# Kernel tuning notes

Hardware: AMD Instinct MI355X
Metric: run time of the kernel (lower is better)

Reference implementation:

```python
import jax, jax.numpy as jnp
import numpy as np

N_NODES = 100000
N_EDGES = 1600000
D = 128
D_FF = 2 * D
BN_EPS = 1e-5


def setup_inputs() -> dict:
    key = jax.random.key(0)
    ks = jax.random.split(key, 16)
    s = lambda k, shp, fan: jax.random.normal(k, shp, jnp.float32) / np.float32(np.sqrt(fan))
    return {
        "x": jax.random.normal(ks[0], (N_NODES, D), jnp.float32),
        "edge_attr": jax.random.normal(ks[1], (N_EDGES, D), jnp.float32),
        "w1g": s(ks[2], (D, D), D),
        "b1g": jnp.zeros((D,), jnp.float32),
        "w2g": s(ks[3], (D, D), D),
        "b2g": jnp.zeros((D,), jnp.float32),
        "bn1_g": jax.random.uniform(ks[4], (D,), jnp.float32, 0.5, 1.5),
        "bn1_b": 0.1 * jax.random.normal(ks[5], (D,), jnp.float32),
        "ff_w1": s(ks[6], (D, D_FF), D),
        "ff_b1": jnp.zeros((D_FF,), jnp.float32),
        "ff_w2": s(ks[7], (D_FF, D), D_FF),
        "ff_b2": jnp.zeros((D,), jnp.float32),
        "bn2_g": jax.random.uniform(ks[8], (D,), jnp.float32, 0.5, 1.5),
        "bn2_b": 0.1 * jax.random.normal(ks[9], (D,), jnp.float32),
        "edge_index": jax.random.randint(ks[10], (2, N_EDGES), 0, N_NODES, jnp.int64 if jax.config.jax_enable_x64 else jnp.int32),
    }


def _batchnorm(h, gamma, beta):
    # training-mode BatchNorm1d: per-batch (node-axis) stats, biased variance
    mean = h.mean(axis=0)
    var = ((h - mean) ** 2).mean(axis=0)
    return gamma * (h - mean) * jax.lax.rsqrt(var + BN_EPS) + beta


def reference(x, edge_attr, w1g, b1g, w2g, b2g, bn1_g, bn1_b,
              ff_w1, ff_b1, ff_w2, ff_b2, bn2_g, bn2_b, edge_index):
    src, dst = edge_index[0], edge_index[1]
    # GINEConv message: relu(x_j + e_ij), scatter-sum into target nodes
    msg = jax.nn.relu(x[src] + edge_attr)                      # [E, D]
    agg = jax.ops.segment_sum(msg, dst, num_segments=N_NODES)  # [N, D]
    h = x + agg                                                # (1+eps)*x with eps=0
    # gin_nn: Linear -> ReLU -> Linear
    h = jax.nn.relu(h @ w1g + b1g) @ w2g + b2g
    h = jax.nn.relu(h)                                         # post-conv relu; dropout=identity (eval)
    h = x + h                                                  # residual
    h = _batchnorm(h, bn1_g, bn1_b)                            # norm1_local
    ff = jax.nn.relu(h @ ff_w1 + ff_b1) @ ff_w2 + ff_b2        # FFN block (dropouts identity)
    h = h + ff
    h = _batchnorm(h, bn2_g, bn2_b)                            # norm2
    return h
```

## Files before the change

kernel.cpp:

```cpp
#include <hip/hip_runtime.h>
#include <hip/hip_bf16.h>

#define NN 100000
#define NE 1600000
#define DD 128
#define DFF 256
#define BN_EPS 1e-5f
#define NND ((size_t)NN * DD)
#define NB_SCAN 391
#define NTILE 6250

typedef __attribute__((ext_vector_type(8))) short short8;
typedef __attribute__((ext_vector_type(4))) float f32x4;
typedef __attribute__((ext_vector_type(4))) unsigned short us4;

static __device__ __forceinline__ unsigned short f2bf(float f) {
  union { float f; unsigned u; } v; v.f = f;
  unsigned r = v.u + 0x7fffu + ((v.u >> 16) & 1u);
  return (unsigned short)(r >> 16);
}
static __device__ __forceinline__ float bf2f(unsigned short h) {
  union { unsigned u; float f; } v; v.u = ((unsigned)h) << 16;
  return v.f;
}

__global__ __launch_bounds__(256) void k_prep_misc(const float* __restrict__ x,
    unsigned short* __restrict__ xbf,
    const float* __restrict__ w1g, const float* __restrict__ w2g,
    const float* __restrict__ ffw1, const float* __restrict__ ffw2,
    unsigned short* __restrict__ w1t, unsigned short* __restrict__ w2t,
    unsigned short* __restrict__ fw1t, unsigned short* __restrict__ fw2t) {
  int b = blockIdx.x;
  if (b < 6250) {
    size_t base = ((size_t)b * 256u + threadIdx.x) * 8;
    const f32x4* xp = reinterpret_cast<const f32x4*>(x + base);
    f32x4 a0 = xp[0], a1 = xp[1];
    short8 o;
#pragma unroll
    for (int j = 0; j < 4; ++j) o[j] = (short)f2bf(a0[j]);
#pragma unroll
    for (int j = 0; j < 4; ++j) o[4 + j] = (short)f2bf(a1[j]);
    *reinterpret_cast<short8*>(xbf + base) = o;
  } else {
    int i = (b - 6250) * 256 + threadIdx.x;
    if (i < 16384) { int c = i & 127, k = i >> 7; w1t[c * 128 + k] = f2bf(w1g[k * 128 + c]); }
    else if (i < 32768) { i -= 16384; int c = i & 127, k = i >> 7; w2t[c * 128 + k] = f2bf(w2g[k * 128 + c]); }
    else if (i < 65536) { i -= 32768; int c = i & 255, k = i >> 8; fw1t[c * 128 + k] = f2bf(ffw1[k * 256 + c]); }
    else if (i < 98304) { i -= 65536; int c = i & 127, k = i >> 7; fw2t[c * 256 + k] = f2bf(ffw2[k * 128 + c]); }
  }
}

__global__ __launch_bounds__(256) void k_hist(const int* __restrict__ ei,
                                              int* __restrict__ cnt) {
  int e = blockIdx.x * 256 + threadIdx.x;
  if (e >= NE) return;
  atomicAdd(&cnt[ei[NE + e]], 1);
}

__global__ __launch_bounds__(256) void k_scan1(const int* __restrict__ cnt,
                                               int* __restrict__ bsum) {
  __shared__ int sh[256];
  int n = blockIdx.x * 256 + threadIdx.x;
  sh[threadIdx.x] = (n < NN) ? cnt[n] : 0;
  __syncthreads();
  for (int off = 128; off > 0; off >>= 1) {
    if (threadIdx.x < off) sh[threadIdx.x] += sh[threadIdx.x + off];
    __syncthreads();
  }
  if (threadIdx.x == 0) bsum[blockIdx.x] = sh[0];
}

__global__ __launch_bounds__(512) void k_scan2(const int* __restrict__ bsum,
                                               int* __restrict__ bpre,
                                               int* __restrict__ rs) {
  __shared__ int sh[512];
  int t = threadIdx.x;
  int v = (t < NB_SCAN) ? bsum[t] : 0;
  sh[t] = v;
  __syncthreads();
  for (int off = 1; off < 512; off <<= 1) {
    int u = (t >= off) ? sh[t - off] : 0;
    __syncthreads();
    sh[t] += u;
    __syncthreads();
  }
  if (t < NB_SCAN) bpre[t] = sh[t] - v;
  if (t == NB_SCAN - 1) rs[NN] = sh[t];
}

__global__ __launch_bounds__(256) void k_scan3(int* __restrict__ rs,
                                               const int* __restrict__ bpre,
                                               int* __restrict__ cursor) {
  __shared__ int sh[256];
  int n = blockIdx.x * 256 + threadIdx.x;
  int t = threadIdx.x;
  int v = (n < NN) ? rs[n] : 0;
  sh[t] = v;
  __syncthreads();
  for (int off = 1; off < 256; off <<= 1) {
    int u = (t >= off) ? sh[t - off] : 0;
    __syncthreads();
    sh[t] += u;
    __syncthreads();
  }
  if (n < NN) {
    int ex = bpre[blockIdx.x] + sh[t] - v;
    rs[n] = ex;
    cursor[n] = ex;
  }
}

__global__ __launch_bounds__(256) void k_scatter(const int* __restrict__ ei,
                                                 int* __restrict__ cursor,
                                                 int2* __restrict__ el2) {
  int e = blockIdx.x * 256 + threadIdx.x;
  if (e >= NE) return;
  int s = ei[e], d = ei[NE + e];
  int p = atomicAdd(&cursor[d], 1);
  el2[p] = make_int2(e, s);
}

__global__ __launch_bounds__(256) void k_gather(
    const unsigned short* __restrict__ xbf, const float* __restrict__ ea,
    const int* __restrict__ rs, const int2* __restrict__ el2,
    unsigned short* __restrict__ h0) {
  int n = blockIdx.x * 8 + (threadIdx.x >> 5);
  int q = threadIdx.x & 31;
  int beg = rs[n], end = rs[n + 1];
  f32x4 acc = (f32x4){0.f, 0.f, 0.f, 0.f};
  int2 E0 = make_int2(0, 0), E1 = E0, E2 = E0, E3 = E0;
  int i = beg;
  if (i     < end) E0 = el2[i];
  if (i + 1 < end) E1 = el2[i + 1];
  if (i + 2 < end) E2 = el2[i + 2];
  if (i + 3 < end) E3 = el2[i + 3];
  for (; i + 4 <= end; i += 4) {
    f32x4 ev0 = *(reinterpret_cast<const f32x4*>(ea + (size_t)E0.x * DD) + q);
    us4  xv0 = *reinterpret_cast<const us4*>(xbf + (size_t)E0.y * DD + q * 4);
    f32x4 ev1 = *(reinterpret_cast<const f32x4*>(ea + (size_t)E1.x * DD) + q);
    us4  xv1 = *reinterpret_cast<const us4*>(xbf + (size_t)E1.y * DD + q * 4);
    f32x4 ev2 = *(reinterpret_cast<const f32x4*>(ea + (size_t)E2.x * DD) + q);
    us4  xv2 = *reinterpret_cast<const us4*>(xbf + (size_t)E2.y * DD + q * 4);
    f32x4 ev3 = *(reinterpret_cast<const f32x4*>(ea + (size_t)E3.x * DD) + q);
    us4  xv3 = *reinterpret_cast<const us4*>(xbf + (size_t)E3.y * DD + q * 4);
    int2 N0 = E0, N1 = E1, N2 = E2, N3 = E3;
    if (i + 4 < end) N0 = el2[i + 4];
    if (i + 5 < end) N1 = el2[i + 5];
    if (i + 6 < end) N2 = el2[i + 6];
    if (i + 7 < end) N3 = el2[i + 7];
#pragma unroll
    for (int c = 0; c < 4; ++c) {
      float m0 = bf2f((unsigned short)xv0[c]) + ev0[c];
      acc[c] += (m0 > 0.f) ? m0 : 0.f;
      float m1 = bf2f((unsigned short)xv1[c]) + ev1[c];
      acc[c] += (m1 > 0.f) ? m1 : 0.f;
      float m2 = bf2f((unsigned short)xv2[c]) + ev2[c];
      acc[c] += (m2 > 0.f) ? m2 : 0.f;
      float m3 = bf2f((unsigned short)xv3[c]) + ev3[c];
      acc[c] += (m3 > 0.f) ? m3 : 0.f;
    }
    E0 = N0; E1 = N1; E2 = N2; E3 = N3;
  }
  if (i < end) {
    f32x4 ev = *(reinterpret_cast<const f32x4*>(ea + (size_t)E0.x * DD) + q);
    us4  xv = *reinterpret_cast<const us4*>(xbf + (size_t)E0.y * DD + q * 4);
#pragma unroll
    for (int c = 0; c < 4; ++c) {
      float m = bf2f((unsigned short)xv[c]) + ev[c];
      acc[c] += (m > 0.f) ? m : 0.f;
    }
  }
  if (i + 1 < end) {
    f32x4 ev = *(reinterpret_cast<const f32x4*>(ea + (size_t)E1.x * DD) + q);
    us4  xv = *reinterpret_cast<const us4*>(xbf + (size_t)E1.y * DD + q * 4);
#pragma unroll
    for (int c = 0; c < 4; ++c) {
      float m = bf2f((unsigned short)xv[c]) + ev[c];
      acc[c] += (m > 0.f) ? m : 0.f;
    }
  }
  if (i + 2 < end) {
    f32x4 ev = *(reinterpret_cast<const f32x4*>(ea + (size_t)E2.x * DD) + q);
    us4  xv = *reinterpret_cast<const us4*>(xbf + (size_t)E2.y * DD + q * 4);
#pragma unroll
    for (int c = 0; c < 4; ++c) {
      float m = bf2f((unsigned short)xv[c]) + ev[c];
      acc[c] += (m > 0.f) ? m : 0.f;
    }
  }
  us4 xs = *reinterpret_cast<const us4*>(xbf + (size_t)n * DD + q * 4);
  union { unsigned short us[4]; unsigned long long u; } pk;
#pragma unroll
  for (int c = 0; c < 4; ++c) pk.us[c] = f2bf(bf2f((unsigned short)xs[c]) + acc[c]);
  *reinterpret_cast<unsigned long long*>(h0 + (size_t)n * DD + q * 4) = pk.u;
}

#define TR1 136
__global__ __launch_bounds__(256) void k_mlp1(const unsigned short* __restrict__ A,
    const unsigned short* __restrict__ W1T, const float* __restrict__ b1,
    const unsigned short* __restrict__ W2T, const float* __restrict__ b2,
    const float* __restrict__ x, float* __restrict__ O, float* __restrict__ stats) {
  __shared__ unsigned short tr[4][16 * TR1];
  __shared__ float lds_s[128], lds_q[128];
  if (threadIdx.x < 128) { lds_s[threadIdx.x] = 0.f; lds_q[threadIdx.x] = 0.f; }
  int lane = threadIdx.x & 63, w = threadIdx.x >> 6;
  int tile = blockIdx.x * 4 + w;
  int l15 = lane & 15, g = lane >> 4;
  int row0 = tile * 16;
  __syncthreads();
  if (tile < NTILE) {
    f32x4 acc[8];
#pragma unroll
    for (int ct = 0; ct < 8; ++ct) {
      float b = b1[ct * 16 + l15];
      acc[ct] = (f32x4){b, b, b, b};
    }
    short8 a[4];
#pragma unroll
    for (int kt = 0; kt < 4; ++kt)
      a[kt] = *reinterpret_cast<const short8*>(A + (size_t)(row0 + l15) * DD + kt * 32 + g * 8);
#pragma unroll
    for (int kt = 0; kt < 4; ++kt) {
      int k0 = kt * 32 + g * 8;
#pragma unroll
      for (int ct = 0; ct < 8; ++ct) {
        int c = ct * 16 + l15;
        short8 b = *reinterpret_cast<const short8*>(W1T + (size_t)c * DD + k0);
        acc[ct] = __builtin_amdgcn_mfma_f32_16x16x32_bf16(a[kt], b, acc[ct], 0, 0, 0);
      }
    }
#pragma unroll
    for (int ct = 0; ct < 8; ++ct) {
#pragma unroll
      for (int r = 0; r < 4; ++r) {
        float v = acc[ct][r];
        v = v > 0.f ? v : 0.f;
        tr[w][(g * 4 + r) * TR1 + ct * 16 + l15] = f2bf(v);
      }
    }
  }
  __syncthreads();
  if (tile < NTILE) {
    short8 a2[4];
#pragma unroll
    for (int kt = 0; kt < 4; ++kt)
      a2[kt] = *reinterpret_cast<const short8*>(&tr[w][l15 * TR1 + kt * 32 + g * 8]);
    f32x4 acc2[8];
#pragma unroll
    for (int ct = 0; ct < 8; ++ct) {
      float b = b2[ct * 16 + l15];
      acc2[ct] = (f32x4){b, b, b, b};
    }
#pragma unroll
    for (int kt = 0; kt < 4; ++kt) {
      int k0 = kt * 32 + g * 8;
#pragma unroll
      for (int ct = 0; ct < 8; ++ct) {
        int c = ct * 16 + l15;
        short8 b = *reinterpret_cast<const short8*>(W2T + (size_t)c * DD + k0);
        acc2[ct] = __builtin_amdgcn_mfma_f32_16x16x32_bf16(a2[kt], b, acc2[ct], 0, 0, 0);
      }
    }
#pragma unroll
    for (int ct = 0; ct < 8; ++ct) {
      int c = ct * 16 + l15;
      float s = 0.f, q = 0.f;
#pragma unroll
      for (int r = 0; r < 4; ++r) {
        int row = row0 + g * 4 + r;
        float v = acc2[ct][r];
        v = v > 0.f ? v : 0.f;
        v += x[(size_t)row * DD + c];
        O[(size_t)row * DD + c] = v;
        s += v; q += v * v;
      }
      s += __shfl_xor(s, 16); s += __shfl_xor(s, 32);
      q += __shfl_xor(q, 16); q += __shfl_xor(q, 32);
      if (g == 0) { atomicAdd(&lds_s[c], s); atomicAdd(&lds_q[c], q); }
    }
  }
  __syncthreads();
  if (threadIdx.x < 128) {
    atomicAdd(&stats[threadIdx.x], lds_s[threadIdx.x]);
    atomicAdd(&stats[128 + threadIdx.x], lds_q[threadIdx.x]);
  }
}

__global__ void k_bnfin(const float* __restrict__ st, const float* __restrict__ gm,
                        const float* __restrict__ bt, float* __restrict__ par) {
  int c = threadIdx.x;
  float mean = st[c] * (1.f / NN);
  float var = st[128 + c] * (1.f / NN) - mean * mean;
  float sc = gm[c] * rsqrtf(var + BN_EPS);
  par[c] = sc;
  par[128 + c] = bt[c] - mean * sc;
}

#define TR2 264
__global__ __launch_bounds__(256) void k_mlp2(const float* __restrict__ H,
    const float* __restrict__ par, const unsigned short* __restrict__ FW1T,
    const float* __restrict__ fb1, const unsigned short* __restrict__ FW2T,
    const float* __restrict__ fb2, float* __restrict__ O, float* __restrict__ stats) {
  __shared__ unsigned short tr[4][16 * TR2];
  __shared__ float lds_s[128], lds_q[128];
  if (threadIdx.x < 128) { lds_s[threadIdx.x] = 0.f; lds_q[threadIdx.x] = 0.f; }
  int lane = threadIdx.x & 63, w = threadIdx.x >> 6;
  int tile = blockIdx.x * 4 + w;
  int l15 = lane & 15, g = lane >> 4;
  int row0 = tile * 16;
  __syncthreads();
  if (tile < NTILE) {
    const float* arow = H + (size_t)(row0 + l15) * DD;
    short8 a1[4];
#pragma unroll
    for (int kt = 0; kt < 4; ++kt) {
      int k0 = kt * 32 + g * 8;
      f32x4 u0 = *reinterpret_cast<const f32x4*>(arow + k0);
      f32x4 u1 = *reinterpret_cast<const f32x4*>(arow + k0 + 4);
      f32x4 sc0 = *reinterpret_cast<const f32x4*>(par + k0);
      f32x4 sc1 = *reinterpret_cast<const f32x4*>(par + k0 + 4);
      f32x4 sh0 = *reinterpret_cast<const f32x4*>(par + 128 + k0);
      f32x4 sh1 = *reinterpret_cast<const f32x4*>(par + 128 + k0 + 4);
      short8 af;
#pragma unroll
      for (int j = 0; j < 4; ++j) af[j] = (short)f2bf(sc0[j] * u0[j] + sh0[j]);
#pragma unroll
      for (int j = 0; j < 4; ++j) af[4 + j] = (short)f2bf(sc1[j] * u1[j] + sh1[j]);
      a1[kt] = af;
    }
    f32x4 acc1[16];
#pragma unroll
    for (int ct = 0; ct < 16; ++ct) {
      float b = fb1[ct * 16 + l15];
      acc1[ct] = (f32x4){b, b, b, b};
    }
#pragma unroll
    for (int kt = 0; kt < 4; ++kt) {
      int k0 = kt * 32 + g * 8;
#pragma unroll
      for (int ct = 0; ct < 16; ++ct) {
        int c = ct * 16 + l15;
        short8 b = *reinterpret_cast<const short8*>(FW1T + (size_t)c * DD + k0);
        acc1[ct] = __builtin_amdgcn_mfma_f32_16x16x32_bf16(a1[kt], b, acc1[ct], 0, 0, 0);
      }
    }
#pragma unroll
    for (int ct = 0; ct < 16; ++ct) {
#pragma unroll
      for (int r = 0; r < 4; ++r) {
        float v = acc1[ct][r];
        v = v > 0.f ? v : 0.f;
        tr[w][(g * 4 + r) * TR2 + ct * 16 + l15] = f2bf(v);
      }
    }
  }
  __syncthreads();
  if (tile < NTILE) {
    short8 a2[8];
#pragma unroll
    for (int kt = 0; kt < 8; ++kt)
      a2[kt] = *reinterpret_cast<const short8*>(&tr[w][l15 * TR2 + kt * 32 + g * 8]);
    f32x4 acc2[8];
#pragma unroll
    for (int ct = 0; ct < 8; ++ct) {
      float b = fb2[ct * 16 + l15];
      acc2[ct] = (f32x4){b, b, b, b};
    }
#pragma unroll 2
    for (int kt = 0; kt < 8; ++kt) {
      int k0 = kt * 32 + g * 8;
#pragma unroll
      for (int ct = 0; ct < 8; ++ct) {
        int c = ct * 16 + l15;
        short8 b = *reinterpret_cast<const short8*>(FW2T + (size_t)c * DFF + k0);
        acc2[ct] = __builtin_amdgcn_mfma_f32_16x16x32_bf16(a2[kt], b, acc2[ct], 0, 0, 0);
      }
    }
#pragma unroll
    for (int ct = 0; ct < 8; ++ct) {
      int c = ct * 16 + l15;
      float sc = par[c], sh = par[128 + c];
      float s = 0.f, q = 0.f;
#pragma unroll
      for (int r = 0; r < 4; ++r) {
        int row = row0 + g * 4 + r;
        float h1v = sc * O[(size_t)row * DD + c] + sh;
        float v = acc2[ct][r] + h1v;
        O[(size_t)row * DD + c] = v;
        s += v; q += v * v;
      }
      s += __shfl_xor(s, 16); s += __shfl_xor(s, 32);
      q += __shfl_xor(q, 16); q += __shfl_xor(q, 32);
      if (g == 0) { atomicAdd(&lds_s[c], s); atomicAdd(&lds_q[c], q); }
    }
  }
  __syncthreads();
  if (threadIdx.x < 128) {
    atomicAdd(&stats[threadIdx.x], lds_s[threadIdx.x]);
    atomicAdd(&stats[128 + threadIdx.x], lds_q[threadIdx.x]);
  }
}

__global__ __launch_bounds__(256) void k_bnfinal(float* __restrict__ h,
    const float* __restrict__ st, const float* __restrict__ gm,
    const float* __restrict__ bt) {
  size_t base = ((size_t)blockIdx.x * 256u + threadIdx.x) * 4;
  int c0 = (int)(base & 127);
  f32x4 v = *reinterpret_cast<f32x4*>(h + base);
#pragma unroll
  for (int j = 0; j < 4; ++j) {
    int c = c0 + j;
    float mean = st[c] * (1.f / NN);
    float var = st[128 + c] * (1.f / NN) - mean * mean;
    float sc = gm[c] * rsqrtf(var + BN_EPS);
    float sh = bt[c] - mean * sc;
    v[j] = sc * v[j] + sh;
  }
  *reinterpret_cast<f32x4*>(h + base) = v;
}

extern "C" void kernel_launch(void* const* d_in, const int* in_sizes, int n_in,
                              void* d_out, int out_size, void* d_ws, size_t ws_size,
                              hipStream_t stream) {
  const float* x    = (const float*)d_in[0];
  const float* ea   = (const float*)d_in[1];
  const float* w1g  = (const float*)d_in[2];
  const float* b1g  = (const float*)d_in[3];
  const float* w2g  = (const float*)d_in[4];
  const float* b2g  = (const float*)d_in[5];
  const float* bn1g = (const float*)d_in[6];
  const float* bn1b = (const float*)d_in[7];
  const float* ffw1 = (const float*)d_in[8];
  const float* ffb1 = (const float*)d_in[9];
  const float* ffw2 = (const float*)d_in[10];
  const float* ffb2 = (const float*)d_in[11];
  const float* bn2g = (const float*)d_in[12];
  const float* bn2b = (const float*)d_in[13];
  const int*   eidx = (const int*)d_in[14];
  float* out = (float*)d_out;

  char* ws = (char*)d_ws;
  int2* el2    = (int2*)(ws);
  int*  rs     = (int*)(ws + 12800000);
  int*  cursor = (int*)(ws + 13200128);
  int*  bsum   = (int*)(ws + 13600128);
  int*  bpre   = (int*)(ws + 13601728);
  float* stats = (float*)(ws + 13603328);
  float* par   = (float*)(ws + 13605376);
  unsigned short* w1t  = (unsigned short*)(ws + 13607424);
  unsigned short* w2t  = w1t + 16384;
  unsigned short* fw1t = w2t + 16384;
  unsigned short* fw2t = fw1t + 32768;
  unsigned short* xbf  = (unsigned short*)(ws + 13804032);
  unsigned short* hbf  = (unsigned short*)(ws + 39404032);

  hipMemsetAsync(rs, 0, (NN + 1) * 4, stream);
  hipMemsetAsync(stats, 0, 512 * 4, stream);

  k_prep_misc<<<6634, 256, 0, stream>>>(x, xbf, w1g, w2g, ffw1, ffw2,
                                        w1t, w2t, fw1t, fw2t);

  k_hist<<<6250, 256, 0, stream>>>(eidx, rs);
  k_scan1<<<NB_SCAN, 256, 0, stream>>>(rs, bsum);
  k_scan2<<<1, 512, 0, stream>>>(bsum, bpre, rs);
  k_scan3<<<NB_SCAN, 256, 0, stream>>>(rs, bpre, cursor);
  k_scatter<<<6250, 256, 0, stream>>>(eidx, cursor, el2);

  k_gather<<<12500, 256, 0, stream>>>(xbf, ea, rs, el2, hbf);

  k_mlp1<<<1563, 256, 0, stream>>>(hbf, w1t, b1g, w2t, b2g, x, out, stats);
  k_bnfin<<<1, 128, 0, stream>>>(stats, bn1g, bn1b, par);
  k_mlp2<<<1563, 256, 0, stream>>>(out, par, fw1t, ffb1, fw2t, ffb2, out, stats + 256);
  k_bnfinal<<<12500, 256, 0, stream>>>(out, stats + 256, bn2g, bn2b);
}
```

Measured before the change: 722.0 us.

## Stage MLP weights in swizzled LDS, loop tiles per block, fuse hist into prep

The MLP kernels now copy the bf16 weight matrices once per block into LDS with an XOR swizzle, and each wave processes four 16-row tiles. The grid shrinks from 1563 to 391 blocks so the weight load is spread over more work. The histogram kernel is merged into the prep launch, the stats memset moves into k_scan2, and the residual in mlp1 reads bf16 x instead of fp32 x. The costs are higher LDS use (lower occupancy), fewer blocks on the device, and a small precision loss in the residual term.

```diff
diff --git a/kernel.cpp b/kernel.cpp
--- a/kernel.cpp
+++ b/kernel.cpp
@@ -29,7 +29,8 @@
     const float* __restrict__ w1g, const float* __restrict__ w2g,
     const float* __restrict__ ffw1, const float* __restrict__ ffw2,
     unsigned short* __restrict__ w1t, unsigned short* __restrict__ w2t,
-    unsigned short* __restrict__ fw1t, unsigned short* __restrict__ fw2t) {
+    unsigned short* __restrict__ fw1t, unsigned short* __restrict__ fw2t,
+    const int* __restrict__ ei, int* __restrict__ cnt) {
   int b = blockIdx.x;
   if (b < 6250) {
     size_t base = ((size_t)b * 256u + threadIdx.x) * 8;
@@ -41,20 +42,16 @@
 #pragma unroll
     for (int j = 0; j < 4; ++j) o[4 + j] = (short)f2bf(a1[j]);
     *reinterpret_cast<short8*>(xbf + base) = o;
-  } else {
+  } else if (b < 6634) {
     int i = (b - 6250) * 256 + threadIdx.x;
     if (i < 16384) { int c = i & 127, k = i >> 7; w1t[c * 128 + k] = f2bf(w1g[k * 128 + c]); }
     else if (i < 32768) { i -= 16384; int c = i & 127, k = i >> 7; w2t[c * 128 + k] = f2bf(w2g[k * 128 + c]); }
     else if (i < 65536) { i -= 32768; int c = i & 255, k = i >> 8; fw1t[c * 128 + k] = f2bf(ffw1[k * 256 + c]); }
     else if (i < 98304) { i -= 65536; int c = i & 127, k = i >> 7; fw2t[c * 256 + k] = f2bf(ffw2[k * 128 + c]); }
-  }
-}
-
-__global__ __launch_bounds__(256) void k_hist(const int* __restrict__ ei,
-                                              int* __restrict__ cnt) {
-  int e = blockIdx.x * 256 + threadIdx.x;
-  if (e >= NE) return;
-  atomicAdd(&cnt[ei[NE + e]], 1);
+  } else {
+    int e = (b - 6634) * 256 + threadIdx.x;
+    if (e < NE) atomicAdd(&cnt[ei[NE + e]], 1);
+  }
 }
 
 __global__ __launch_bounds__(256) void k_scan1(const int* __restrict__ cnt,
@@ -72,9 +69,11 @@
 
 __global__ __launch_bounds__(512) void k_scan2(const int* __restrict__ bsum,
                                                int* __restrict__ bpre,
-                                               int* __restrict__ rs) {
+                                               int* __restrict__ rs,
+                                               float* __restrict__ stats) {
   __shared__ int sh[512];
   int t = threadIdx.x;
+  stats[t] = 0.f;
   int v = (t < NB_SCAN) ? bsum[t] : 0;
   sh[t] = v;
   __syncthreads();
@@ -199,90 +198,103 @@
 __global__ __launch_bounds__(256) void k_mlp1(const unsigned short* __restrict__ A,
     const unsigned short* __restrict__ W1T, const float* __restrict__ b1,
     const unsigned short* __restrict__ W2T, const float* __restrict__ b2,
-    const float* __restrict__ x, float* __restrict__ O, float* __restrict__ stats) {
+    const unsigned short* __restrict__ xbf, float* __restrict__ O,
+    float* __restrict__ stats) {
+  __shared__ unsigned short w1s[16384];
+  __shared__ unsigned short w2s[16384];
   __shared__ unsigned short tr[4][16 * TR1];
   __shared__ float lds_s[128], lds_q[128];
-  if (threadIdx.x < 128) { lds_s[threadIdx.x] = 0.f; lds_q[threadIdx.x] = 0.f; }
-  int lane = threadIdx.x & 63, w = threadIdx.x >> 6;
-  int tile = blockIdx.x * 4 + w;
+  int t = threadIdx.x;
+  if (t < 128) { lds_s[t] = 0.f; lds_q[t] = 0.f; }
+  {
+    const short8* s1 = reinterpret_cast<const short8*>(W1T);
+    const short8* s2 = reinterpret_cast<const short8*>(W2T);
+    for (int i = t; i < 2048; i += 256) {
+      int byte = i * 16;
+      int c = byte >> 8;
+      int sb = byte ^ ((c & 7) << 4);
+      *reinterpret_cast<short8*>(reinterpret_cast<char*>(w1s) + sb) = s1[i];
+      *reinterpret_cast<short8*>(reinterpret_cast<char*>(w2s) + sb) = s2[i];
+    }
+  }
+  __syncthreads();
+  int lane = t & 63, w = t >> 6;
   int l15 = lane & 15, g = lane >> 4;
-  int row0 = tile * 16;
-  __syncthreads();
-  if (tile < NTILE) {
-    f32x4 acc[8];
-#pragma unroll
-    for (int ct = 0; ct < 8; ++ct) {
-      float b = b1[ct * 16 + l15];
-      acc[ct] = (f32x4){b, b, b, b};
-    }
-    short8 a[4];
-#pragma unroll
-    for (int kt = 0; kt < 4; ++kt)
-      a[kt] = *reinterpret_cast<const short8*>(A + (size_t)(row0 + l15) * DD + kt * 32 + g * 8);
-#pragma unroll
-    for (int kt = 0; kt < 4; ++kt) {
-      int k0 = kt * 32 + g * 8;
+  for (int tt = 0; tt < 4; ++tt) {
+    int tile = blockIdx.x * 16 + w * 4 + tt;
+    bool valid = tile < NTILE;
+    int row0 = tile * 16;
+    if (valid) {
+      short8 a[4];
+#pragma unroll
+      for (int kt = 0; kt < 4; ++kt)
+        a[kt] = *reinterpret_cast<const short8*>(A + (size_t)(row0 + l15) * DD + kt * 32 + g * 8);
+      f32x4 acc[8];
+#pragma unroll
+      for (int ct = 0; ct < 8; ++ct) { float b = b1[ct * 16 + l15]; acc[ct] = (f32x4){b, b, b, b}; }
+#pragma unroll
+      for (int kt = 0; kt < 4; ++kt) {
+        int k0 = kt * 32 + g * 8;
+#pragma unroll
+        for (int ct = 0; ct < 8; ++ct) {
+          int c = ct * 16 + l15;
+          int byte = ((c << 8) + k0 * 2) ^ ((c & 7) << 4);
+          short8 b = *reinterpret_cast<const short8*>(reinterpret_cast<const char*>(w1s) + byte);
+          acc[ct] = __builtin_amdgcn_mfma_f32_16x16x32_bf16(a[kt], b, acc[ct], 0, 0, 0);
+        }
+      }
+#pragma unroll
+      for (int ct = 0; ct < 8; ++ct)
+#pragma unroll
+        for (int r = 0; r < 4; ++r) {
+          float v = acc[ct][r];
+          v = v > 0.f ? v : 0.f;
+          tr[w][(g * 4 + r) * TR1 + ct * 16 + l15] = f2bf(v);
+        }
+    }
+    __syncthreads();
+    if (valid) {
+      short8 a2[4];
+#pragma unroll
+      for (int kt = 0; kt < 4; ++kt)
+        a2[kt] = *reinterpret_cast<const short8*>(&tr[w][l15 * TR1 + kt * 32 + g * 8]);
+      f32x4 acc2[8];
+#pragma unroll
+      for (int ct = 0; ct < 8; ++ct) { float b = b2[ct * 16 + l15]; acc2[ct] = (f32x4){b, b, b, b}; }
+#pragma unroll
+      for (int kt = 0; kt < 4; ++kt) {
+        int k0 = kt * 32 + g * 8;
+#pragma unroll
+        for (int ct = 0; ct < 8; ++ct) {
+          int c = ct * 16 + l15;
+          int byte = ((c << 8) + k0 * 2) ^ ((c & 7) << 4);
+          short8 b = *reinterpret_cast<const short8*>(reinterpret_cast<const char*>(w2s) + byte);
+          acc2[ct] = __builtin_amdgcn_mfma_f32_16x16x32_bf16(a2[kt], b, acc2[ct], 0, 0, 0);
+        }
+      }
 #pragma unroll
       for (int ct = 0; ct < 8; ++ct) {
         int c = ct * 16 + l15;
-        short8 b = *reinterpret_cast<const short8*>(W1T + (size_t)c * DD + k0);
-        acc[ct] = __builtin_amdgcn_mfma_f32_16x16x32_bf16(a[kt], b, acc[ct], 0, 0, 0);
-      }
-    }
-#pragma unroll
-    for (int ct = 0; ct < 8; ++ct) {
-#pragma unroll
-      for (int r = 0; r < 4; ++r) {
-        float v = acc[ct][r];
-        v = v > 0.f ? v : 0.f;
-        tr[w][(g * 4 + r) * TR1 + ct * 16 + l15] = f2bf(v);
-      }
-    }
-  }
-  __syncthreads();
-  if (tile < NTILE) {
-    short8 a2[4];
-#pragma unroll
-    for (int kt = 0; kt < 4; ++kt)
-      a2[kt] = *reinterpret_cast<const short8*>(&tr[w][l15 * TR1 + kt * 32 + g * 8]);
-    f32x4 acc2[8];
-#pragma unroll
-    for (int ct = 0; ct < 8; ++ct) {
-      float b = b2[ct * 16 + l15];
-      acc2[ct] = (f32x4){b, b, b, b};
-    }
-#pragma unroll
-    for (int kt = 0; kt < 4; ++kt) {
-      int k0 = kt * 32 + g * 8;
-#pragma unroll
-      for (int ct = 0; ct < 8; ++ct) {
-        int c = ct * 16 + l15;
-        short8 b = *reinterpret_cast<const short8*>(W2T + (size_t)c * DD + k0);
-        acc2[ct] = __builtin_amdgcn_mfma_f32_16x16x32_bf16(a2[kt], b, acc2[ct], 0, 0, 0);
-      }
-    }
-#pragma unroll
-    for (int ct = 0; ct < 8; ++ct) {
-      int c = ct * 16 + l15;
-      float s = 0.f, q = 0.f;
-#pragma unroll
-      for (int r = 0; r < 4; ++r) {
-        int row = row0 + g * 4 + r;
-        float v = acc2[ct][r];
-        v = v > 0.f ? v : 0.f;
-        v += x[(size_t)row * DD + c];
-        O[(size_t)row * DD + c] = v;
-        s += v; q += v * v;
-      }
-      s += __shfl_xor(s, 16); s += __shfl_xor(s, 32);
-      q += __shfl_xor(q, 16); q += __shfl_xor(q, 32);
-      if (g == 0) { atomicAdd(&lds_s[c], s); atomicAdd(&lds_q[c], q); }
-    }
-  }
-  __syncthreads();
-  if (threadIdx.x < 128) {
-    atomicAdd(&stats[threadIdx.x], lds_s[threadIdx.x]);
-    atomicAdd(&stats[128 + threadIdx.x], lds_q[threadIdx.x]);
+        float s = 0.f, q = 0.f;
+#pragma unroll
+        for (int r = 0; r < 4; ++r) {
+          int row = row0 + g * 4 + r;
+          float v = acc2[ct][r];
+          v = v > 0.f ? v : 0.f;
+          v += bf2f(xbf[(size_t)row * DD + c]);
+          O[(size_t)row * DD + c] = v;
+          s += v; q += v * v;
+        }
+        s += __shfl_xor(s, 16); s += __shfl_xor(s, 32);
+        q += __shfl_xor(q, 16); q += __shfl_xor(q, 32);
+        if (g == 0) { atomicAdd(&lds_s[c], s); atomicAdd(&lds_q[c], q); }
+      }
+    }
+    __syncthreads();
+  }
+  if (t < 128) {
+    atomicAdd(&stats[t], lds_s[t]);
+    atomicAdd(&stats[128 + t], lds_q[t]);
   }
 }
 
@@ -301,103 +313,111 @@
     const float* __restrict__ par, const unsigned short* __restrict__ FW1T,
     const float* __restrict__ fb1, const unsigned short* __restrict__ FW2T,
     const float* __restrict__ fb2, float* __restrict__ O, float* __restrict__ stats) {
+  __shared__ unsigned short fw1s[32768];
   __shared__ unsigned short tr[4][16 * TR2];
   __shared__ float lds_s[128], lds_q[128];
-  if (threadIdx.x < 128) { lds_s[threadIdx.x] = 0.f; lds_q[threadIdx.x] = 0.f; }
-  int lane = threadIdx.x & 63, w = threadIdx.x >> 6;
-  int tile = blockIdx.x * 4 + w;
+  int t = threadIdx.x;
+  if (t < 128) { lds_s[t] = 0.f; lds_q[t] = 0.f; }
+  {
+    const short8* s1 = reinterpret_cast<const short8*>(FW1T);
+    for (int i = t; i < 4096; i += 256) {
+      int byte = i * 16;
+      int c = byte >> 8;
+      int sb = byte ^ ((c & 7) << 4);
+      *reinterpret_cast<short8*>(reinterpret_cast<char*>(fw1s) + sb) = s1[i];
+    }
+  }
+  __syncthreads();
+  int lane = t & 63, w = t >> 6;
   int l15 = lane & 15, g = lane >> 4;
-  int row0 = tile * 16;
-  __syncthreads();
-  if (tile < NTILE) {
-    const float* arow = H + (size_t)(row0 + l15) * DD;
-    short8 a1[4];
-#pragma unroll
-    for (int kt = 0; kt < 4; ++kt) {
-      int k0 = kt * 32 + g * 8;
-      f32x4 u0 = *reinterpret_cast<const f32x4*>(arow + k0);
-      f32x4 u1 = *reinterpret_cast<const f32x4*>(arow + k0 + 4);
-      f32x4 sc0 = *reinterpret_cast<const f32x4*>(par + k0);
-      f32x4 sc1 = *reinterpret_cast<const f32x4*>(par + k0 + 4);
-      f32x4 sh0 = *reinterpret_cast<const f32x4*>(par + 128 + k0);
-      f32x4 sh1 = *reinterpret_cast<const f32x4*>(par + 128 + k0 + 4);
-      short8 af;
-#pragma unroll
-      for (int j = 0; j < 4; ++j) af[j] = (short)f2bf(sc0[j] * u0[j] + sh0[j]);
-#pragma unroll
-      for (int j = 0; j < 4; ++j) af[4 + j] = (short)f2bf(sc1[j] * u1[j] + sh1[j]);
-      a1[kt] = af;
-    }
-    f32x4 acc1[16];
-#pragma unroll
-    for (int ct = 0; ct < 16; ++ct) {
-      float b = fb1[ct * 16 + l15];
-      acc1[ct] = (f32x4){b, b, b, b};
-    }
-#pragma unroll
-    for (int kt = 0; kt < 4; ++kt) {
-      int k0 = kt * 32 + g * 8;
-#pragma unroll
-      for (int ct = 0; ct < 16; ++ct) {
-        int c = ct * 16 + l15;
-        short8 b = *reinterpret_cast<const short8*>(FW1T + (size_t)c * DD + k0);
-        acc1[ct] = __builtin_amdgcn_mfma_f32_16x16x32_bf16(a1[kt], b, acc1[ct], 0, 0, 0);
-      }
-    }
-#pragma unroll
-    for (int ct = 0; ct < 16; ++ct) {
-#pragma unroll
-      for (int r = 0; r < 4; ++r) {
-        float v = acc1[ct][r];
-        v = v > 0.f ? v : 0.f;
-        tr[w][(g * 4 + r) * TR2 + ct * 16 + l15] = f2bf(v);
-      }
-    }
-  }
-  __syncthreads();
-  if (tile < NTILE) {
-    short8 a2[8];
-#pragma unroll
-    for (int kt = 0; kt < 8; ++kt)
-      a2[kt] = *reinterpret_cast<const short8*>(&tr[w][l15 * TR2 + kt * 32 + g * 8]);
-    f32x4 acc2[8];
-#pragma unroll
-    for (int ct = 0; ct < 8; ++ct) {
-      float b = fb2[ct * 16 + l15];
-      acc2[ct] = (f32x4){b, b, b, b};
-    }
+  for (int tt = 0; tt < 4; ++tt) {
+    int tile = blockIdx.x * 16 + w * 4 + tt;
+    bool valid = tile < NTILE;
+    int row0 = tile * 16;
+    if (valid) {
+      const float* arow = H + (size_t)(row0 + l15) * DD;
+      short8 a1[4];
+#pragma unroll
+      for (int kt = 0; kt < 4; ++kt) {
+        int k0 = kt * 32 + g * 8;
+        f32x4 u0 = *reinterpret_cast<const f32x4*>(arow + k0);
+        f32x4 u1 = *reinterpret_cast<const f32x4*>(arow + k0 + 4);
+        f32x4 sc0 = *reinterpret_cast<const f32x4*>(par + k0);
+        f32x4 sc1 = *reinterpret_cast<const f32x4*>(par + k0 + 4);
+        f32x4 sh0 = *reinterpret_cast<const f32x4*>(par + 128 + k0);
+        f32x4 sh1 = *reinterpret_cast<const f32x4*>(par + 128 + k0 + 4);
+        short8 af;
+#pragma unroll
+        for (int j = 0; j < 4; ++j) af[j] = (short)f2bf(sc0[j] * u0[j] + sh0[j]);
+#pragma unroll
+        for (int j = 0; j < 4; ++j) af[4 + j] = (short)f2bf(sc1[j] * u1[j] + sh1[j]);
+        a1[kt] = af;
+      }
+      f32x4 acc1[16];
+#pragma unroll
+      for (int ct = 0; ct < 16; ++ct) { float b = fb1[ct * 16 + l15]; acc1[ct] = (f32x4){b, b, b, b}; }
+#pragma unroll
+      for (int kt = 0; kt < 4; ++kt) {
+        int k0 = kt * 32 + g * 8;
+#pragma unroll
+        for (int ct = 0; ct < 16; ++ct) {
+          int c = ct * 16 + l15;
+          int byte = ((c << 8) + k0 * 2) ^ ((c & 7) << 4);
+          short8 b = *reinterpret_cast<const short8*>(reinterpret_cast<const char*>(fw1s) + byte);
+          acc1[ct] = __builtin_amdgcn_mfma_f32_16x16x32_bf16(a1[kt], b, acc1[ct], 0, 0, 0);
+        }
+      }
+#pragma unroll
+      for (int ct = 0; ct < 16; ++ct)
+#pragma unroll
+        for (int r = 0; r < 4; ++r) {
+          float v = acc1[ct][r];
+          v = v > 0.f ? v : 0.f;
+          tr[w][(g * 4 + r) * TR2 + ct * 16 + l15] = f2bf(v);
+        }
+    }
+    __syncthreads();
+    if (valid) {
+      short8 a2[8];
+#pragma unroll
+      for (int kt = 0; kt < 8; ++kt)
+        a2[kt] = *reinterpret_cast<const short8*>(&tr[w][l15 * TR2 + kt * 32 + g * 8]);
+      f32x4 acc2[8];
+#pragma unroll
+      for (int ct = 0; ct < 8; ++ct) { float b = fb2[ct * 16 + l15]; acc2[ct] = (f32x4){b, b, b, b}; }
 #pragma unroll 2
-    for (int kt = 0; kt < 8; ++kt) {
-      int k0 = kt * 32 + g * 8;
+      for (int kt = 0; kt < 8; ++kt) {
+        int k0 = kt * 32 + g * 8;
+#pragma unroll
+        for (int ct = 0; ct < 8; ++ct) {
+          int c = ct * 16 + l15;
+          short8 b = *reinterpret_cast<const short8*>(FW2T + (size_t)c * DFF + k0);
+          acc2[ct] = __builtin_amdgcn_mfma_f32_16x16x32_bf16(a2[kt], b, acc2[ct], 0, 0, 0);
+        }
+      }
 #pragma unroll
       for (int ct = 0; ct < 8; ++ct) {
         int c = ct * 16 + l15;
-        short8 b = *reinterpret_cast<const short8*>(FW2T + (size_t)c * DFF + k0);
-        acc2[ct] = __builtin_amdgcn_mfma_f32_16x16x32_bf16(a2[kt], b, acc2[ct], 0, 0, 0);
-      }
-    }
-#pragma unroll
-    for (int ct = 0; ct < 8; ++ct) {
-      int c = ct * 16 + l15;
-      float sc = par[c], sh = par[128 + c];
-      float s = 0.f, q = 0.f;
-#pragma unroll
-      for (int r = 0; r < 4; ++r) {
-        int row = row0 + g * 4 + r;
-        float h1v = sc * O[(size_t)row * DD + c] + sh;
-        float v = acc2[ct][r] + h1v;
-        O[(size_t)row * DD + c] = v;
-        s += v; q += v * v;
-      }
-      s += __shfl_xor(s, 16); s += __shfl_xor(s, 32);
-      q += __shfl_xor(q, 16); q += __shfl_xor(q, 32);
-      if (g == 0) { atomicAdd(&lds_s[c], s); atomicAdd(&lds_q[c], q); }
-    }
-  }
-  __syncthreads();
-  if (threadIdx.x < 128) {
-    atomicAdd(&stats[threadIdx.x], lds_s[threadIdx.x]);
-    atomicAdd(&stats[128 + threadIdx.x], lds_q[threadIdx.x]);
+        float sc = par[c], sh = par[128 + c];
+        float s = 0.f, q = 0.f;
+#pragma unroll
+        for (int r = 0; r < 4; ++r) {
+          int row = row0 + g * 4 + r;
+          float h1v = sc * O[(size_t)row * DD + c] + sh;
+          float v = acc2[ct][r] + h1v;
+          O[(size_t)row * DD + c] = v;
+          s += v; q += v * v;
+        }
+        s += __shfl_xor(s, 16); s += __shfl_xor(s, 32);
+        q += __shfl_xor(q, 16); q += __shfl_xor(q, 32);
+        if (g == 0) { atomicAdd(&lds_s[c], s); atomicAdd(&lds_q[c], q); }
+      }
+    }
+    __syncthreads();
+  }
+  if (t < 128) {
+    atomicAdd(&stats[t], lds_s[t]);
+    atomicAdd(&stats[128 + t], lds_q[t]);
   }
 }
 
@@ -455,21 +475,19 @@
   unsigned short* hbf  = (unsigned short*)(ws + 39404032);
 
   hipMemsetAsync(rs, 0, (NN + 1) * 4, stream);
-  hipMemsetAsync(stats, 0, 512 * 4, stream);
-
-  k_prep_misc<<<6634, 256, 0, stream>>>(x, xbf, w1g, w2g, ffw1, ffw2,
-                                        w1t, w2t, fw1t, fw2t);
-
-  k_hist<<<6250, 256, 0, stream>>>(eidx, rs);
+
+  k_prep_misc<<<12884, 256, 0, stream>>>(x, xbf, w1g, w2g, ffw1, ffw2,
+                                         w1t, w2t, fw1t, fw2t, eidx, rs);
+
   k_scan1<<<NB_SCAN, 256, 0, stream>>>(rs, bsum);
-  k_scan2<<<1, 512, 0, stream>>>(bsum, bpre, rs);
+  k_scan2<<<1, 512, 0, stream>>>(bsum, bpre, rs, stats);
   k_scan3<<<NB_SCAN, 256, 0, stream>>>(rs, bpre, cursor);
   k_scatter<<<6250, 256, 0, stream>>>(eidx, cursor, el2);
 
   k_gather<<<12500, 256, 0, stream>>>(xbf, ea, rs, el2, hbf);
 
-  k_mlp1<<<1563, 256, 0, stream>>>(hbf, w1t, b1g, w2t, b2g, x, out, stats);
+  k_mlp1<<<391, 256, 0, stream>>>(hbf, w1t, b1g, w2t, b2g, xbf, out, stats);
   k_bnfin<<<1, 128, 0, stream>>>(stats, bn1g, bn1b, par);
-  k_mlp2<<<1563, 256, 0, stream>>>(out, par, fw1t, ffb1, fw2t, ffb2, out, stats + 256);
+  k_mlp2<<<391, 256, 0, stream>>>(out, par, fw1t, ffb1, fw2t, ffb2, out, stats + 256);
   k_bnfinal<<<12500, 256, 0, stream>>>(out, stats + 256, bn2g, bn2b);
 }
```

Result: slower. 745.7 us (+3.3%).
